# Kernel optimization log

Measured on AMD Instinct MI355X. Metric: run time of the kernel, lower is better.

## Reference

```python
import jax, jax.numpy as jnp
import numpy as np

B_, N_, D_ = 2, 2048, 512
E_ = 2 * D_          # d_inner = expand * dim
S_ = 16              # d_state
K_ = 4               # d_conv
R_ = 32              # dt_rank = ceil(dim/16)
C_ = 512             # cond_dim


def setup_inputs() -> dict:
    key = jax.random.key(0)
    ks = jax.random.split(key, 12)
    r = lambda i, sh, s=0.02: jax.random.normal(ks[i], sh, dtype=jnp.float32) * s
    return {
        "x": jax.random.normal(ks[0], (B_, N_, D_), dtype=jnp.float32),
        "cond": jax.random.normal(ks[1], (B_, C_), dtype=jnp.float32),
        "ln_g": jnp.ones((D_,), jnp.float32),
        "ln_b": jnp.zeros((D_,), jnp.float32),
        "W_in": r(2, (D_, 2 * E_)),            # in_proj (no bias)
        "conv_w": r(3, (E_, K_), 0.1),          # depthwise causal conv
        "conv_b": jnp.zeros((E_,), jnp.float32),
        "W_x": r(4, (E_, R_ + 2 * S_)),         # x_proj -> dt,B,C
        "W_dt": r(5, (R_, E_), 0.1),
        "b_dt": jnp.full((E_,), -4.6, jnp.float32),  # softplus(-4.6)~0.01
        "A_log": jnp.log(jnp.broadcast_to(jnp.arange(1, S_ + 1, dtype=jnp.float32), (E_, S_))),
        "D_skip": jnp.ones((E_,), jnp.float32),
        "W_out": r(6, (E_, D_)),                # out_proj (no bias)
        "film_gw": r(7, (C_, D_)),
        "film_gb": jnp.ones((D_,), jnp.float32),
        "film_bw": r(8, (C_, D_)),
        "film_bb": jnp.zeros((D_,), jnp.float32),
    }


def reference(x, cond, ln_g, ln_b, W_in, conv_w, conv_b, W_x, W_dt, b_dt,
              A_log, D_skip, W_out, film_gw, film_gb, film_bw, film_bb):
    # --- LayerNorm ---
    mu = x.mean(-1, keepdims=True)
    var = ((x - mu) ** 2).mean(-1, keepdims=True)
    xn = (x - mu) * jax.lax.rsqrt(var + 1e-5) * ln_g + ln_b

    # --- Mamba ---
    xz = xn @ W_in                                  # [B,N,2E]
    u, z = jnp.split(xz, 2, axis=-1)                # [B,N,E] each
    # causal depthwise conv1d (kernel K_), unrolled over small K
    up = jnp.pad(u, ((0, 0), (K_ - 1, 0), (0, 0)))
    uc = conv_b + sum(up[:, k:k + N_, :] * conv_w[:, k] for k in range(K_))
    uc = jax.nn.silu(uc)                            # [B,N,E]

    x_dbl = uc @ W_x                                # [B,N,R+2S]
    dt, Bm, Cm = jnp.split(x_dbl, [R_, R_ + S_], axis=-1)
    delta = jax.nn.softplus(dt @ W_dt + b_dt)       # [B,N,E]

    A = -jnp.exp(A_log)                             # [E,S]
    dA = jnp.exp(delta[..., None] * A)              # [B,N,E,S]
    dBu = (delta * uc)[..., None] * Bm[:, :, None, :]  # [B,N,E,S]

    def step(h, ins):
        dA_t, dBu_t, C_t = ins                      # [B,E,S],[B,E,S],[B,S]
        h = dA_t * h + dBu_t
        y = jnp.einsum('bes,bs->be', h, C_t)
        return h, y

    h0 = jnp.zeros((x.shape[0], E_, S_), dtype=x.dtype)
    _, ys = jax.lax.scan(step, h0,
                         (dA.swapaxes(0, 1), dBu.swapaxes(0, 1), Cm.swapaxes(0, 1)))
    y = ys.swapaxes(0, 1) + D_skip * uc             # [B,N,E]
    y = y * jax.nn.silu(z)
    out = y @ W_out                                 # [B,N,D]

    # --- FiLM ---
    gamma = cond @ film_gw + film_gb                # [B,D]
    beta = cond @ film_bw + film_bb
    return gamma[:, None, :] * out + beta[:, None, :]
```

## Files before the change

### kernel.cpp

```cpp
#include <hip/hip_runtime.h>
#include <hip/hip_bf16.h>
#include <math.h>

#define B_ 2
#define N_ 2048
#define D_ 512
#define E_ 1024
#define S_ 16
#define R_ 32
#define C_ 512
#define CH_ 32
#define NC_ 64
#define FC_ 128

using short8 = __attribute__((ext_vector_type(8))) short;
using f32x4  = __attribute__((ext_vector_type(4))) float;
using f32x16 = __attribute__((ext_vector_type(16))) float;

__device__ __forceinline__ short f2bf(float f) {
    union { float f; unsigned u; } x; x.f = f;
    unsigned r = (x.u + 0x7fffu + ((x.u >> 16) & 1u)) >> 16;
    return (short)r;
}
__device__ __forceinline__ float bf2f(short s) {
    union { unsigned u; float f; } x;
    x.u = ((unsigned)(unsigned short)s) << 16;
    return x.f;
}
__device__ __forceinline__ void gl_lds16(const void* g, void* l) {
    __builtin_amdgcn_global_load_lds((const __attribute__((address_space(1))) void*)g,
                                     (__attribute__((address_space(3))) void*)l, 16, 0, 0);
}

__device__ __forceinline__ void transpose32(const float* __restrict__ W, short* __restrict__ Wt,
                                            int K, int N, int bx, int by, float (*t)[33], int tid) {
    int n0 = bx * 32, k0 = by * 32;
    int c = tid & 31, rr0 = tid >> 5;
#pragma unroll
    for (int rr = rr0; rr < 32; rr += 8)
        t[rr][c] = W[(size_t)(k0 + rr) * N + n0 + c];
    __syncthreads();
#pragma unroll
    for (int rr = rr0; rr < 32; rr += 8)
        Wt[(size_t)(n0 + rr) * K + k0 + c] = f2bf(t[c][rr]);
}

__global__ __launch_bounds__(256) void prep1_kernel(
    const float* __restrict__ x, short* __restrict__ xnb,
    const float* __restrict__ lng, const float* __restrict__ lnb,
    const float* __restrict__ W_in, short* __restrict__ Wint) {
    __shared__ __align__(16) float smem[32 * 33];
    int bid = blockIdx.x;
    int tid = threadIdx.x;
    if (bid < 1024) {
        int t = bid * 4 + (tid >> 6);
        int lane = tid & 63;
        const float* src = x + (size_t)t * D_ + lane * 8;
        float4 v0 = *(const float4*)src;
        float4 v1 = *(const float4*)(src + 4);
        float s = v0.x + v0.y + v0.z + v0.w + v1.x + v1.y + v1.z + v1.w;
        float s2 = v0.x * v0.x;
        s2 = fmaf(v0.y, v0.y, s2); s2 = fmaf(v0.z, v0.z, s2); s2 = fmaf(v0.w, v0.w, s2);
        s2 = fmaf(v1.x, v1.x, s2); s2 = fmaf(v1.y, v1.y, s2);
        s2 = fmaf(v1.z, v1.z, s2); s2 = fmaf(v1.w, v1.w, s2);
#pragma unroll
        for (int o = 32; o >= 1; o >>= 1) {
            s += __shfl_xor(s, o);
            s2 += __shfl_xor(s2, o);
        }
        float mu = s * (1.f / (float)D_);
        float var = s2 * (1.f / (float)D_) - mu * mu;
        float rs = rsqrtf(var + 1e-5f);
        float4 g0 = *(const float4*)(lng + lane * 8);
        float4 g1 = *(const float4*)(lng + lane * 8 + 4);
        float4 b0 = *(const float4*)(lnb + lane * 8);
        float4 b1 = *(const float4*)(lnb + lane * 8 + 4);
        short8 o;
        o[0] = f2bf((v0.x - mu) * rs * g0.x + b0.x);
        o[1] = f2bf((v0.y - mu) * rs * g0.y + b0.y);
        o[2] = f2bf((v0.z - mu) * rs * g0.z + b0.z);
        o[3] = f2bf((v0.w - mu) * rs * g0.w + b0.w);
        o[4] = f2bf((v1.x - mu) * rs * g1.x + b1.x);
        o[5] = f2bf((v1.y - mu) * rs * g1.y + b1.y);
        o[6] = f2bf((v1.z - mu) * rs * g1.z + b1.z);
        o[7] = f2bf((v1.w - mu) * rs * g1.w + b1.w);
        *(short8*)(xnb + (size_t)t * D_ + lane * 8) = o;
    } else {
        int r = bid - 1024;
        transpose32(W_in, Wint, 512, 2048, r % 64, r / 64, (float(*)[33])smem, tid);
    }
}

__global__ __launch_bounds__(256) void gemm1_hybrid(
    const short* __restrict__ A, const short* __restrict__ Bt, short* __restrict__ Cb,
    const float* __restrict__ W_out, short* __restrict__ Woutt,
    const float* __restrict__ W_x, short* __restrict__ Wxt,
    const float* __restrict__ W_dt, short* __restrict__ Wdtt,
    const float* __restrict__ cond,
    const float* __restrict__ gw, const float* __restrict__ gb,
    const float* __restrict__ bw, const float* __restrict__ bb,
    float* __restrict__ gamma, float* __restrict__ beta) {
    __shared__ __align__(16) char smem[32768];
    int bid = blockIdx.x;
    int tid = threadIdx.x;
    if (bid < 512) {
        constexpr int BM = 128, BN = 128, BK = 64;
        constexpr int N = 2048, K = 512;
        short* As = (short*)smem;
        short* Bs = As + BM * BK;
        int lane = tid & 63, w = tid >> 6;
        int wr = w >> 1, wc = w & 1;
        int swz = (bid & 7) * 64 + (bid >> 3);
        int m0 = (swz >> 4) * BM, n0 = (swz & 15) * BN;
        int lr = lane >> 3, lc = lane & 7;
        f32x16 acc[2][2];
#pragma unroll
        for (int i = 0; i < 2; i++)
#pragma unroll
            for (int j = 0; j < 2; j++)
#pragma unroll
                for (int r = 0; r < 16; r++) acc[i][j][r] = 0.f;
        int l31 = lane & 31, hk = (lane >> 5) * 8;
        for (int k0 = 0; k0 < K; k0 += BK) {
            __syncthreads();
#pragma unroll
            for (int ch = w; ch < BM / 8; ch += 4)
                gl_lds16(&A[(size_t)(m0 + ch * 8 + lr) * K + k0 + lc * 8], &As[ch * 512]);
#pragma unroll
            for (int ch = w; ch < BN / 8; ch += 4)
                gl_lds16(&Bt[(size_t)(n0 + ch * 8 + lr) * K + k0 + lc * 8], &Bs[ch * 512]);
            __syncthreads();
#pragma unroll
            for (int kk = 0; kk < 4; kk++) {
                short8 a[2], b[2];
#pragma unroll
                for (int i = 0; i < 2; i++)
                    a[i] = *(const short8*)&As[(wr * 64 + i * 32 + l31) * BK + kk * 16 + hk];
#pragma unroll
                for (int j = 0; j < 2; j++)
                    b[j] = *(const short8*)&Bs[(wc * 64 + j * 32 + l31) * BK + kk * 16 + hk];
#pragma unroll
                for (int i = 0; i < 2; i++)
#pragma unroll
                    for (int j = 0; j < 2; j++)
                        acc[i][j] = __builtin_amdgcn_mfma_f32_32x32x16_bf16(a[i], b[j], acc[i][j], 0, 0, 0);
            }
        }
        int rbase = 4 * (lane >> 5);
#pragma unroll
        for (int i = 0; i < 2; i++)
#pragma unroll
            for (int j = 0; j < 2; j++) {
                int col = n0 + wc * 64 + j * 32 + l31;
#pragma unroll
                for (int r = 0; r < 16; r++) {
                    int row = m0 + wr * 64 + i * 32 + rbase + (r & 3) + 8 * (r >> 2);
                    Cb[(size_t)row * N + col] = f2bf(acc[i][j][r]);
                }
            }
    } else if (bid < 520) {
        float* cs = (float*)smem;
        float* red = (float*)smem + 1024;
        int d0 = (bid - 512) * 64;
#pragma unroll
        for (int i = tid; i < 2 * C_ / 4; i += 256) {
            int b = i >> 7;
            int c4 = (i & 127) * 4;
            *(float4*)&cs[b * C_ + c4] = *(const float4*)(cond + (size_t)b * C_ + c4);
        }
        __syncthreads();
        int dl = tid & 63, ks = tid >> 6;
        int d = d0 + dl;
        float g0 = 0.f, g1 = 0.f, bt0 = 0.f, bt1 = 0.f;
#pragma unroll 4
        for (int k = ks * 128; k < ks * 128 + 128; k++) {
            float wg = gw[(size_t)k * D_ + d];
            float wb = bw[(size_t)k * D_ + d];
            float c0 = cs[k], c1 = cs[C_ + k];
            g0 = fmaf(c0, wg, g0);
            g1 = fmaf(c1, wg, g1);
            bt0 = fmaf(c0, wb, bt0);
            bt1 = fmaf(c1, wb, bt1);
        }
        red[(ks * 64 + dl) * 4 + 0] = g0; red[(ks * 64 + dl) * 4 + 1] = g1;
        red[(ks * 64 + dl) * 4 + 2] = bt0; red[(ks * 64 + dl) * 4 + 3] = bt1;
        __syncthreads();
        if (ks == 0) {
            float s0 = 0.f, s1 = 0.f, s2 = 0.f, s3 = 0.f;
#pragma unroll
            for (int q = 0; q < 4; q++) {
                s0 += red[(q * 64 + dl) * 4 + 0]; s1 += red[(q * 64 + dl) * 4 + 1];
                s2 += red[(q * 64 + dl) * 4 + 2]; s3 += red[(q * 64 + dl) * 4 + 3];
            }
            float gbv = gb[d], bbv = bb[d];
            gamma[d] = s0 + gbv;
            gamma[D_ + d] = s1 + gbv;
            beta[d] = s2 + bbv;
            beta[D_ + d] = s3 + bbv;
        }
    } else if (bid < 1032) {
        int r = bid - 520;
        transpose32(W_out, Woutt, 1024, 512, r % 16, r / 16, (float(*)[33])smem, tid);
    } else if (bid < 1096) {
        int r = bid - 1032;
        transpose32(W_x, Wxt, 1024, 64, r % 2, r / 2, (float(*)[33])smem, tid);
    } else {
        int r = bid - 1096;
        transpose32(W_dt, Wdtt, 32, 1024, r, 0, (float(*)[33])smem, tid);
    }
}

template <int BM, int BN>
__global__ __launch_bounds__(256) void gemm2_kernel(
    const short* __restrict__ A, const short* __restrict__ Bt, float* __restrict__ Cf,
    int M, int N, int K,
    const float* __restrict__ gamma, const float* __restrict__ beta) {
    constexpr int BK = 64;
    constexpr int WM = BM / 2, WN = BN / 2;
    constexpr int MR = WM / 32, NR = WN / 32;
    __shared__ __align__(16) short As[BM * BK];
    __shared__ __align__(16) short Bs[BN * BK];
    int tid = threadIdx.x;
    int lane = tid & 63, w = tid >> 6;
    int wr = w >> 1, wc = w & 1;
    int lid = blockIdx.x;
    int chunk = gridDim.x >> 3;
    int swz = (lid & 7) * chunk + (lid >> 3);
    int ntiles = N / BN;
    int m0 = (swz / ntiles) * BM, n0 = (swz % ntiles) * BN;
    int lr = lane >> 3, lc = lane & 7;

    f32x16 acc[MR][NR];
#pragma unroll
    for (int i = 0; i < MR; i++)
#pragma unroll
        for (int j = 0; j < NR; j++)
#pragma unroll
            for (int r = 0; r < 16; r++) acc[i][j][r] = 0.f;

    int l31 = lane & 31, hk = (lane >> 5) * 8;

    for (int k0 = 0; k0 < K; k0 += BK) {
        __syncthreads();
#pragma unroll
        for (int ch = w; ch < BM / 8; ch += 4)
            gl_lds16(&A[(size_t)(m0 + ch * 8 + lr) * K + k0 + lc * 8], &As[ch * 512]);
#pragma unroll
        for (int ch = w; ch < BN / 8; ch += 4)
            gl_lds16(&Bt[(size_t)(n0 + ch * 8 + lr) * K + k0 + lc * 8], &Bs[ch * 512]);
        __syncthreads();
#pragma unroll
        for (int kk = 0; kk < 4; kk++) {
            short8 a[MR], b[NR];
#pragma unroll
            for (int i = 0; i < MR; i++)
                a[i] = *(const short8*)&As[(wr * WM + i * 32 + l31) * BK + kk * 16 + hk];
#pragma unroll
            for (int j = 0; j < NR; j++)
                b[j] = *(const short8*)&Bs[(wc * WN + j * 32 + l31) * BK + kk * 16 + hk];
#pragma unroll
            for (int i = 0; i < MR; i++)
#pragma unroll
                for (int j = 0; j < NR; j++)
                    acc[i][j] = __builtin_amdgcn_mfma_f32_32x32x16_bf16(a[i], b[j], acc[i][j], 0, 0, 0);
        }
    }
    int rbase = 4 * (lane >> 5);
    int bi = m0 >> 11;
#pragma unroll
    for (int i = 0; i < MR; i++)
#pragma unroll
        for (int j = 0; j < NR; j++) {
            int col = n0 + wc * WN + j * 32 + l31;
            float gm = gamma[bi * D_ + col];
            float bt = beta[bi * D_ + col];
#pragma unroll
            for (int r = 0; r < 16; r++) {
                int row = m0 + wr * WM + i * 32 + rbase + (r & 3) + 8 * (r >> 2);
                Cf[(size_t)row * N + col] = gm * acc[i][j][r] + bt;
            }
        }
}

__global__ __launch_bounds__(512) void mid_kernel(
    const short* __restrict__ xzb, const float* __restrict__ cw, const float* __restrict__ cb,
    const short* __restrict__ Wxt,
    const short* __restrict__ Wdtt,
    const float* __restrict__ bdt, const float* __restrict__ A_log,
    short* __restrict__ ucb, float* __restrict__ xdbl, short* __restrict__ deltab,
    short* __restrict__ hend, float* __restrict__ cumd) {
    constexpr int LDU = 1032;
    __shared__ __align__(16) short u[16 * LDU];
    __shared__ __align__(16) float xd2[2][16 * 68];
    int tid = threadIdx.x;
    int t0 = blockIdx.x * 16;
    int n0 = t0 & (N_ - 1);
    {
        int c8 = (tid & 127) * 8;
        int base = (tid >> 7) * 4;
        float4 wv[8];
        float cbv[8];
#pragma unroll
        for (int j = 0; j < 8; j++) {
            wv[j] = *(const float4*)(cw + (c8 + j) * 4);
            cbv[j] = cb[c8 + j];
        }
        float uf[7][8];
#pragma unroll
        for (int j = 0; j < 7; j++) {
            short8 v = {0, 0, 0, 0, 0, 0, 0, 0};
            if (n0 + base - 3 + j >= 0)
                v = *(const short8*)&xzb[(size_t)(t0 + base - 3 + j) * (2 * E_) + c8];
#pragma unroll
            for (int q = 0; q < 8; q++) uf[j][q] = bf2f(v[q]);
        }
#pragma unroll
        for (int k = 0; k < 4; k++) {
            int n = base + k;
            short8 o;
#pragma unroll
            for (int q = 0; q < 8; q++) {
                float a = fmaf(wv[q].x, uf[k][q],
                          fmaf(wv[q].y, uf[k + 1][q],
                          fmaf(wv[q].z, uf[k + 2][q],
                          fmaf(wv[q].w, uf[k + 3][q], cbv[q]))));
                float v = a / (1.f + __expf(-a));
                o[q] = f2bf(v);
            }
            *(short8*)&ucb[(size_t)(t0 + n) * E_ + c8] = o;
            *(short8*)&u[n * LDU + c8] = o;
        }
    }
    __syncthreads();
    int lane = tid & 63, w = tid >> 6;
    int cg = w & 3, kh = w >> 2;
    int l15 = lane & 15, kq = (lane >> 4) * 8;
    f32x4 acc4 = {0.f, 0.f, 0.f, 0.f};
#pragma unroll 8
    for (int k0 = 0; k0 < 16; k0++) {
        int kk = kh * 512 + k0 * 32;
        short8 af = *(const short8*)&u[l15 * LDU + kk + kq];
        short8 bfr = *(const short8*)&Wxt[(size_t)(cg * 16 + l15) * E_ + kk + kq];
        acc4 = __builtin_amdgcn_mfma_f32_16x16x32_bf16(af, bfr, acc4, 0, 0, 0);
    }
#pragma unroll
    for (int j = 0; j < 4; j++)
        xd2[kh][((lane >> 4) * 4 + j) * 68 + cg * 16 + l15] = acc4[j];
    __syncthreads();
    if (tid < 256) {
        int r = tid >> 4, c4 = (tid & 15) * 4;
        float4 a = *(const float4*)&xd2[0][r * 68 + c4];
        float4 b = *(const float4*)&xd2[1][r * 68 + c4];
        a.x += b.x; a.y += b.y; a.z += b.z; a.w += b.w;
        *(float4*)&xd2[0][r * 68 + c4] = a;
        *(float4*)&xdbl[(size_t)(t0 + r) * 64 + c4] = a;
    }
    __syncthreads();
    {
        float av[8];
        *(float4*)&av[0] = *(const float4*)&xd2[0][l15 * 68 + kq];
        *(float4*)&av[4] = *(const float4*)&xd2[0][l15 * 68 + kq + 4];
        short8 ab;
#pragma unroll
        for (int j = 0; j < 8; j++) ab[j] = f2bf(av[j]);
        int row4 = (lane >> 4) * 4;
#pragma unroll 4
        for (int t = 0; t < 8; t++) {
            int e = w * 128 + t * 16 + l15;
            short8 bb = *(const short8*)&Wdtt[(size_t)e * 32 + kq];
            f32x4 c4v = {0.f, 0.f, 0.f, 0.f};
            c4v = __builtin_amdgcn_mfma_f32_16x16x32_bf16(ab, bb, c4v, 0, 0, 0);
            float bv = bdt[e];
#pragma unroll
            for (int j = 0; j < 4; j++) {
                float xv = c4v[j] + bv;
                float sp = (xv > 20.f) ? xv : log1pf(__expf(xv));
                deltab[(size_t)(t0 + row4 + j) * E_ + e] = f2bf(sp);
            }
        }
    }
    __syncthreads();
#pragma unroll
    for (int half = 0; half < 2; half++) {
        int e = tid + half * 512;
        float Aes[16];
        const float4* al = (const float4*)(A_log + e * 16);
#pragma unroll
        for (int j = 0; j < 4; j++) {
            float4 a = al[j];
            Aes[j * 4 + 0] = -__expf(a.x);
            Aes[j * 4 + 1] = -__expf(a.y);
            Aes[j * 4 + 2] = -__expf(a.z);
            Aes[j * 4 + 3] = -__expf(a.w);
        }
        float h[16];
#pragma unroll
        for (int s = 0; s < 16; s++) h[s] = 0.f;
        float cum = 0.f;
#pragma unroll 2
        for (int n = 0; n < 16; n++) {
            float dv = bf2f(deltab[(size_t)(t0 + n) * E_ + e]);
            float uv = bf2f(u[n * LDU + e]);
            float du = dv * uv;
            cum += dv;
#pragma unroll
            for (int s = 0; s < 16; s++) {
                float dA = __expf(dv * Aes[s]);
                h[s] = fmaf(dA, h[s], du * xd2[0][n * 68 + 32 + s]);
            }
        }
#pragma unroll
        for (int s = 0; s < 16; s++)
            hend[((size_t)blockIdx.x * 16 + s) * E_ + e] = f2bf(h[s]);
        cumd[(size_t)blockIdx.x * E_ + e] = cum;
    }
}

__global__ __launch_bounds__(256) void scan_comb(short* __restrict__ hend,
                                                 const float* __restrict__ cumd,
                                                 const float* __restrict__ A_log) {
    __shared__ float lh[FC_][33];
    __shared__ float lp[FC_][33];
    int blk = blockIdx.x;
    int et = blk & 31;
    int s = (blk >> 5) & 15;
    int b = blk >> 9;
    int e0 = et * 32;
    int tid = threadIdx.x;
    int lane = tid & 63, w = tid >> 6;
    for (int i = tid; i < FC_ * 32; i += 256) {
        int c = i >> 5, e = i & 31;
        lh[c][e] = bf2f(hend[((size_t)((b * FC_ + c) * 16) + s) * E_ + e0 + e]);
        lp[c][e] = cumd[(size_t)(b * FC_ + c) * E_ + e0 + e];
    }
    __syncthreads();
#pragma unroll
    for (int q = 0; q < 8; q++) {
        int e = w * 8 + q;
        float Aes = -__expf(A_log[(e0 + e) * 16 + s]);
        int c0 = 2 * lane, c1 = c0 + 1;
        float A0 = __expf(Aes * lp[c0][e]);
        float B0 = lh[c0][e];
        float A1 = __expf(Aes * lp[c1][e]);
        float B1 = lh[c1][e];
        float A = A1 * A0;
        float Bv = fmaf(A1, B0, B1);
#pragma unroll
        for (int off = 1; off < 64; off <<= 1) {
            float Ap = __shfl_up(A, off);
            float Bp = __shfl_up(Bv, off);
            if (lane >= off) {
                Bv = fmaf(A, Bp, Bv);
                A *= Ap;
            }
        }
        float pB = __shfl_up(Bv, 1);
        if (lane == 0) pB = 0.f;
        lh[c0][e] = pB;
        lh[c1][e] = fmaf(A0, pB, B0);
    }
    __syncthreads();
    for (int i = tid; i < FC_ * 32; i += 256) {
        int c = i >> 5, e = i & 31;
        hend[((size_t)((b * FC_ + c) * 16) + s) * E_ + e0 + e] = f2bf(lh[c][e]);
    }
}

__global__ __launch_bounds__(256) void scan_p3(const short* __restrict__ deltab,
                                               const short* __restrict__ ucb,
                                               const float* __restrict__ xdbl,
                                               const short* __restrict__ xzb,
                                               const float* __restrict__ A_log,
                                               const float* __restrict__ D_skip,
                                               const short* __restrict__ hend,
                                               short* __restrict__ yb) {
    int blk = blockIdx.x;
    int eq = blk & 3;
    int c = (blk >> 2) & (NC_ - 1);
    int b = blk >> 8;
    int tid = threadIdx.x;
    int e = eq * 256 + tid;
    __shared__ float Bsl[CH_][16];
    __shared__ float Csl[CH_][16];
    int base = (b * N_ + c * CH_) * 64;
    for (int i = tid; i < CH_ * 32; i += 256) {
        int n = i >> 5, col = i & 31;
        float v = xdbl[base + n * 64 + R_ + col];
        if (col < 16) Bsl[n][col] = v;
        else Csl[n][col - 16] = v;
    }
    float Aes[16];
    const float4* al = (const float4*)(A_log + e * 16);
#pragma unroll
    for (int j = 0; j < 4; j++) {
        float4 a = al[j];
        Aes[j * 4 + 0] = -__expf(a.x);
        Aes[j * 4 + 1] = -__expf(a.y);
        Aes[j * 4 + 2] = -__expf(a.z);
        Aes[j * 4 + 3] = -__expf(a.w);
    }
    float dsk = D_skip[e];
    float h[16];
    size_t ob = (size_t)((b * FC_ + c * 2) * 16) * E_ + e;
#pragma unroll
    for (int s = 0; s < 16; s++) h[s] = bf2f(hend[ob + (size_t)s * E_]);
    __syncthreads();
    const short* dp = deltab + (size_t)(b * N_ + c * CH_) * E_ + e;
    const short* up = ucb + (size_t)(b * N_ + c * CH_) * E_ + e;
    const short* zp = xzb + (size_t)(b * N_ + c * CH_) * (2 * E_) + E_ + e;
    short* yp = yb + (size_t)(b * N_ + c * CH_) * E_ + e;
#pragma unroll 2
    for (int n = 0; n < CH_; n++) {
        float dv = bf2f(dp[n * E_]);
        float uv = bf2f(up[n * E_]);
        float du = dv * uv;
        float Bl[16], Cl[16];
#pragma unroll
        for (int j = 0; j < 4; j++) {
            *(float4*)&Bl[j * 4] = *(const float4*)&Bsl[n][j * 4];
            *(float4*)&Cl[j * 4] = *(const float4*)&Csl[n][j * 4];
        }
        float y = 0.f;
#pragma unroll
        for (int s = 0; s < 16; s++) {
            float dA = __expf(dv * Aes[s]);
            h[s] = fmaf(dA, h[s], du * Bl[s]);
            y = fmaf(h[s], Cl[s], y);
        }
        float zv = bf2f(zp[n * 2 * E_]);
        float yy = y + dsk * uv;
        yy = yy * (zv / (1.f + __expf(-zv)));
        yp[n * E_] = f2bf(yy);
    }
}

extern "C" void kernel_launch(void* const* d_in, const int* in_sizes, int n_in,
                              void* d_out, int out_size, void* d_ws, size_t ws_size,
                              hipStream_t stream) {
    const float* x       = (const float*)d_in[0];
    const float* cond    = (const float*)d_in[1];
    const float* ln_g    = (const float*)d_in[2];
    const float* ln_b    = (const float*)d_in[3];
    const float* W_in    = (const float*)d_in[4];
    const float* conv_w  = (const float*)d_in[5];
    const float* conv_b  = (const float*)d_in[6];
    const float* W_x     = (const float*)d_in[7];
    const float* W_dt    = (const float*)d_in[8];
    const float* b_dt    = (const float*)d_in[9];
    const float* A_log   = (const float*)d_in[10];
    const float* D_skip  = (const float*)d_in[11];
    const float* W_out   = (const float*)d_in[12];
    const float* film_gw = (const float*)d_in[13];
    const float* film_gb = (const float*)d_in[14];
    const float* film_bw = (const float*)d_in[15];
    const float* film_bb = (const float*)d_in[16];
    float* out = (float*)d_out;

    float* ws = (float*)d_ws;
    float* xdbl  = ws;
    float* gamma = xdbl + 262144;
    float* beta  = gamma + 1024;
    float* cumd  = beta + 1024;
    short* hend  = (short*)(cumd + 262144);
    short* xzb   = hend + 4194304;
    short* ucb   = xzb + 8388608;
    short* deltab = ucb + 4194304;
    short* Wint  = deltab + 4194304;
    short* Woutt = Wint + 1048576;
    short* yb    = Woutt + 524288;
    short* Wxt   = yb + 4194304;
    short* Wdtt  = Wxt + 65536;
    short* xnb   = Wdtt + 32768;

    prep1_kernel<<<2048, 256, 0, stream>>>(x, xnb, ln_g, ln_b, W_in, Wint);

    gemm1_hybrid<<<1128, 256, 0, stream>>>(
        xnb, Wint, xzb, W_out, Woutt, W_x, Wxt, W_dt, Wdtt,
        cond, film_gw, film_gb, film_bw, film_bb, gamma, beta);

    mid_kernel<<<B_ * N_ / 16, 512, 0, stream>>>(
        xzb, conv_w, conv_b, Wxt, Wdtt, b_dt, A_log, ucb, xdbl, deltab, hend, cumd);

    scan_comb<<<B_ * S_ * 32, 256, 0, stream>>>(hend, cumd, A_log);

    scan_p3<<<B_ * NC_ * 4, 256, 0, stream>>>(deltab, ucb, xdbl, xzb, A_log, D_skip, hend, yb);

    gemm2_kernel<64, 64>
        <<<512, 256, 0, stream>>>(
            yb, Woutt, out, B_ * N_, D_, E_, gamma, beta);
}
```

Before: 130.9 us.

## Split chunk scan out of mid kernel and use 16-step chunks with exp2

```diff
diff --git a/kernel.cpp b/kernel.cpp
--- a/kernel.cpp
+++ b/kernel.cpp
@@ -9,13 +9,14 @@
 #define S_ 16
 #define R_ 32
 #define C_ 512
-#define CH_ 32
-#define NC_ 64
 #define FC_ 128
+#define FCH_ 16
 
 using short8 = __attribute__((ext_vector_type(8))) short;
 using f32x4  = __attribute__((ext_vector_type(4))) float;
 using f32x16 = __attribute__((ext_vector_type(16))) float;
+
+#define LOG2E 1.44269504f
 
 __device__ __forceinline__ short f2bf(float f) {
     union { float f; unsigned u; } x; x.f = f;
@@ -286,9 +287,8 @@
     const short* __restrict__ xzb, const float* __restrict__ cw, const float* __restrict__ cb,
     const short* __restrict__ Wxt,
     const short* __restrict__ Wdtt,
-    const float* __restrict__ bdt, const float* __restrict__ A_log,
-    short* __restrict__ ucb, float* __restrict__ xdbl, short* __restrict__ deltab,
-    short* __restrict__ hend, float* __restrict__ cumd) {
+    const float* __restrict__ bdt,
+    short* __restrict__ ucb, float* __restrict__ xdbl, short* __restrict__ deltab) {
     constexpr int LDU = 1032;
     __shared__ __align__(16) short u[16 * LDU];
     __shared__ __align__(16) float xd2[2][16 * 68];
@@ -356,64 +356,83 @@
         *(float4*)&xdbl[(size_t)(t0 + r) * 64 + c4] = a;
     }
     __syncthreads();
-    {
-        float av[8];
-        *(float4*)&av[0] = *(const float4*)&xd2[0][l15 * 68 + kq];
-        *(float4*)&av[4] = *(const float4*)&xd2[0][l15 * 68 + kq + 4];
-        short8 ab;
-#pragma unroll
-        for (int j = 0; j < 8; j++) ab[j] = f2bf(av[j]);
-        int row4 = (lane >> 4) * 4;
+    float av[8];
+    *(float4*)&av[0] = *(const float4*)&xd2[0][l15 * 68 + kq];
+    *(float4*)&av[4] = *(const float4*)&xd2[0][l15 * 68 + kq + 4];
+    short8 ab;
+#pragma unroll
+    for (int j = 0; j < 8; j++) ab[j] = f2bf(av[j]);
+    int row4 = (lane >> 4) * 4;
 #pragma unroll 4
-        for (int t = 0; t < 8; t++) {
-            int e = w * 128 + t * 16 + l15;
-            short8 bb = *(const short8*)&Wdtt[(size_t)e * 32 + kq];
-            f32x4 c4v = {0.f, 0.f, 0.f, 0.f};
-            c4v = __builtin_amdgcn_mfma_f32_16x16x32_bf16(ab, bb, c4v, 0, 0, 0);
-            float bv = bdt[e];
-#pragma unroll
-            for (int j = 0; j < 4; j++) {
-                float xv = c4v[j] + bv;
-                float sp = (xv > 20.f) ? xv : log1pf(__expf(xv));
-                deltab[(size_t)(t0 + row4 + j) * E_ + e] = f2bf(sp);
-            }
-        }
-    }
-    __syncthreads();
-#pragma unroll
-    for (int half = 0; half < 2; half++) {
-        int e = tid + half * 512;
-        float Aes[16];
-        const float4* al = (const float4*)(A_log + e * 16);
+    for (int t = 0; t < 8; t++) {
+        int e = w * 128 + t * 16 + l15;
+        short8 bb = *(const short8*)&Wdtt[(size_t)e * 32 + kq];
+        f32x4 c4v = {0.f, 0.f, 0.f, 0.f};
+        c4v = __builtin_amdgcn_mfma_f32_16x16x32_bf16(ab, bb, c4v, 0, 0, 0);
+        float bv = bdt[e];
 #pragma unroll
         for (int j = 0; j < 4; j++) {
-            float4 a = al[j];
-            Aes[j * 4 + 0] = -__expf(a.x);
-            Aes[j * 4 + 1] = -__expf(a.y);
-            Aes[j * 4 + 2] = -__expf(a.z);
-            Aes[j * 4 + 3] = -__expf(a.w);
-        }
-        float h[16];
-#pragma unroll
-        for (int s = 0; s < 16; s++) h[s] = 0.f;
-        float cum = 0.f;
+            float xv = c4v[j] + bv;
+            float sp = (xv > 20.f) ? xv : log1pf(__expf(xv));
+            deltab[(size_t)(t0 + row4 + j) * E_ + e] = f2bf(sp);
+        }
+    }
+}
+
+__global__ __launch_bounds__(256) void scan_p1(const short* __restrict__ deltab,
+                                               const short* __restrict__ ucb,
+                                               const float* __restrict__ xdbl,
+                                               const float* __restrict__ A_log,
+                                               short* __restrict__ hend,
+                                               float* __restrict__ cumd) {
+    int blk = blockIdx.x;
+    int eq = blk & 3;
+    int c = (blk >> 2) & (FC_ - 1);
+    int b = blk >> 9;
+    int tid = threadIdx.x;
+    int e = eq * 256 + tid;
+    __shared__ float Bsl[FCH_][16];
+    int base = (b * N_ + c * FCH_) * 64;
+    if (tid < FCH_ * 16) {
+        int n = tid >> 4, col = tid & 15;
+        Bsl[n][col] = xdbl[base + n * 64 + R_ + col];
+    }
+    float Aes[16];
+    const float4* al = (const float4*)(A_log + e * 16);
+#pragma unroll
+    for (int j = 0; j < 4; j++) {
+        float4 a = al[j];
+        Aes[j * 4 + 0] = -LOG2E * __expf(a.x);
+        Aes[j * 4 + 1] = -LOG2E * __expf(a.y);
+        Aes[j * 4 + 2] = -LOG2E * __expf(a.z);
+        Aes[j * 4 + 3] = -LOG2E * __expf(a.w);
+    }
+    __syncthreads();
+    float h[16];
+#pragma unroll
+    for (int s = 0; s < 16; s++) h[s] = 0.f;
+    float cum = 0.f;
+    const short* dp = deltab + (size_t)(b * N_ + c * FCH_) * E_ + e;
+    const short* up = ucb + (size_t)(b * N_ + c * FCH_) * E_ + e;
 #pragma unroll 2
-        for (int n = 0; n < 16; n++) {
-            float dv = bf2f(deltab[(size_t)(t0 + n) * E_ + e]);
-            float uv = bf2f(u[n * LDU + e]);
-            float du = dv * uv;
-            cum += dv;
-#pragma unroll
-            for (int s = 0; s < 16; s++) {
-                float dA = __expf(dv * Aes[s]);
-                h[s] = fmaf(dA, h[s], du * xd2[0][n * 68 + 32 + s]);
-            }
-        }
-#pragma unroll
-        for (int s = 0; s < 16; s++)
-            hend[((size_t)blockIdx.x * 16 + s) * E_ + e] = f2bf(h[s]);
-        cumd[(size_t)blockIdx.x * E_ + e] = cum;
-    }
+    for (int n = 0; n < FCH_; n++) {
+        float dv = bf2f(dp[n * E_]);
+        float uv = bf2f(up[n * E_]);
+        float du = dv * uv;
+        cum += dv;
+        float Bl[16];
+#pragma unroll
+        for (int j = 0; j < 4; j++) *(float4*)&Bl[j * 4] = *(const float4*)&Bsl[n][j * 4];
+#pragma unroll
+        for (int s = 0; s < 16; s++) {
+            float dA = exp2f(dv * Aes[s]);
+            h[s] = fmaf(dA, h[s], du * Bl[s]);
+        }
+    }
+    size_t ob = (size_t)((b * FC_ + c) * 16) * E_ + e;
+#pragma unroll
+    for (int s = 0; s < 16; s++) hend[ob + (size_t)s * E_] = f2bf(h[s]);
+    cumd[(size_t)(b * FC_ + c) * E_ + e] = cum;
 }
 
 __global__ __launch_bounds__(256) void scan_comb(short* __restrict__ hend,
@@ -437,11 +456,11 @@
 #pragma unroll
     for (int q = 0; q < 8; q++) {
         int e = w * 8 + q;
-        float Aes = -__expf(A_log[(e0 + e) * 16 + s]);
+        float Aes = -LOG2E * __expf(A_log[(e0 + e) * 16 + s]);
         int c0 = 2 * lane, c1 = c0 + 1;
-        float A0 = __expf(Aes * lp[c0][e]);
+        float A0 = exp2f(Aes * lp[c0][e]);
         float B0 = lh[c0][e];
-        float A1 = __expf(Aes * lp[c1][e]);
+        float A1 = exp2f(Aes * lp[c1][e]);
         float B1 = lh[c1][e];
         float A = A1 * A0;
         float Bv = fmaf(A1, B0, B1);
@@ -476,15 +495,15 @@
                                                short* __restrict__ yb) {
     int blk = blockIdx.x;
     int eq = blk & 3;
-    int c = (blk >> 2) & (NC_ - 1);
-    int b = blk >> 8;
+    int c = (blk >> 2) & (FC_ - 1);
+    int b = blk >> 9;
     int tid = threadIdx.x;
     int e = eq * 256 + tid;
-    __shared__ float Bsl[CH_][16];
-    __shared__ float Csl[CH_][16];
-    int base = (b * N_ + c * CH_) * 64;
-    for (int i = tid; i < CH_ * 32; i += 256) {
-        int n = i >> 5, col = i & 31;
+    __shared__ float Bsl[FCH_][16];
+    __shared__ float Csl[FCH_][16];
+    int base = (b * N_ + c * FCH_) * 64;
+    if (tid < FCH_ * 32) {
+        int n = tid >> 5, col = tid & 31;
         float v = xdbl[base + n * 64 + R_ + col];
         if (col < 16) Bsl[n][col] = v;
         else Csl[n][col - 16] = v;
@@ -494,23 +513,23 @@
 #pragma unroll
     for (int j = 0; j < 4; j++) {
         float4 a = al[j];
-        Aes[j * 4 + 0] = -__expf(a.x);
-        Aes[j * 4 + 1] = -__expf(a.y);
-        Aes[j * 4 + 2] = -__expf(a.z);
-        Aes[j * 4 + 3] = -__expf(a.w);
+        Aes[j * 4 + 0] = -LOG2E * __expf(a.x);
+        Aes[j * 4 + 1] = -LOG2E * __expf(a.y);
+        Aes[j * 4 + 2] = -LOG2E * __expf(a.z);
+        Aes[j * 4 + 3] = -LOG2E * __expf(a.w);
     }
     float dsk = D_skip[e];
     float h[16];
-    size_t ob = (size_t)((b * FC_ + c * 2) * 16) * E_ + e;
+    size_t ob = (size_t)((b * FC_ + c) * 16) * E_ + e;
 #pragma unroll
     for (int s = 0; s < 16; s++) h[s] = bf2f(hend[ob + (size_t)s * E_]);
     __syncthreads();
-    const short* dp = deltab + (size_t)(b * N_ + c * CH_) * E_ + e;
-    const short* up = ucb + (size_t)(b * N_ + c * CH_) * E_ + e;
-    const short* zp = xzb + (size_t)(b * N_ + c * CH_) * (2 * E_) + E_ + e;
-    short* yp = yb + (size_t)(b * N_ + c * CH_) * E_ + e;
+    const short* dp = deltab + (size_t)(b * N_ + c * FCH_) * E_ + e;
+    const short* up = ucb + (size_t)(b * N_ + c * FCH_) * E_ + e;
+    const short* zp = xzb + (size_t)(b * N_ + c * FCH_) * (2 * E_) + E_ + e;
+    short* yp = yb + (size_t)(b * N_ + c * FCH_) * E_ + e;
 #pragma unroll 2
-    for (int n = 0; n < CH_; n++) {
+    for (int n = 0; n < FCH_; n++) {
         float dv = bf2f(dp[n * E_]);
         float uv = bf2f(up[n * E_]);
         float du = dv * uv;
@@ -523,7 +542,7 @@
         float y = 0.f;
 #pragma unroll
         for (int s = 0; s < 16; s++) {
-            float dA = __expf(dv * Aes[s]);
+            float dA = exp2f(dv * Aes[s]);
             h[s] = fmaf(dA, h[s], du * Bl[s]);
             y = fmaf(h[s], Cl[s], y);
         }
@@ -579,11 +598,13 @@
         cond, film_gw, film_gb, film_bw, film_bb, gamma, beta);
 
     mid_kernel<<<B_ * N_ / 16, 512, 0, stream>>>(
-        xzb, conv_w, conv_b, Wxt, Wdtt, b_dt, A_log, ucb, xdbl, deltab, hend, cumd);
+        xzb, conv_w, conv_b, Wxt, Wdtt, b_dt, ucb, xdbl, deltab);
+
+    scan_p1<<<B_ * FC_ * 4, 256, 0, stream>>>(deltab, ucb, xdbl, A_log, hend, cumd);
 
     scan_comb<<<B_ * S_ * 32, 256, 0, stream>>>(hend, cumd, A_log);
 
-    scan_p3<<<B_ * NC_ * 4, 256, 0, stream>>>(deltab, ucb, xdbl, xzb, A_log, D_skip, hend, yb);
+    scan_p3<<<B_ * FC_ * 4, 256, 0, stream>>>(deltab, ucb, xdbl, xzb, A_log, D_skip, hend, yb);
 
     gemm2_kernel<64, 64>
         <<<512, 256, 0, stream>>>(
```

Result: slower. 143.3 us (+9.5%).
